# Kernel optimization log

Hardware: AMD Instinct MI355X
Metric: run time of the kernel (lower is better)

The kernel has to match this reference:

```python
import jax, jax.numpy as jnp
import numpy as np
from jax import lax

B, C_IN, C_OUT, H, W, K, PAD = 4, 64, 64, 96, 96, 3, 1
K2 = K * K


def setup_inputs() -> dict:
    key = jax.random.key(0)
    k1, k2, k3, k4, k5 = jax.random.split(key, 5)
    x = jax.random.normal(k1, (B, C_IN, H, W), jnp.float32)
    offset = jax.random.normal(k2, (B, 2 * K2, H, W), jnp.float32)
    weight = jax.random.normal(k3, (C_OUT, C_IN, K, K), jnp.float32) * 0.05
    mask_weight = jax.random.normal(k4, (K2, C_IN, K, K), jnp.float32) * 0.05
    mask_bias = jax.random.normal(k5, (K2,), jnp.float32) * 0.05
    return {"x": x, "offset": offset, "weight": weight,
            "mask_weight": mask_weight, "mask_bias": mask_bias}


def _deform_conv2d(x, offset, weight, mask):
    # torchvision ordering: per kernel tap k, offset[:, 2k] is dy, offset[:, 2k+1] is dx
    off_y = offset[:, 0::2]  # [B, K2, H, W]
    off_x = offset[:, 1::2]
    ky, kx = jnp.meshgrid(jnp.arange(K), jnp.arange(K), indexing="ij")
    ky = ky.reshape(K2).astype(x.dtype)
    kx = kx.reshape(K2).astype(x.dtype)
    hh = jnp.arange(H, dtype=x.dtype)
    ww = jnp.arange(W, dtype=x.dtype)
    base_y = hh[None, :, None] - PAD + ky[:, None, None]   # [K2, H, 1]
    base_x = ww[None, None, :] - PAD + kx[:, None, None]   # [K2, 1, W]
    py = base_y[None] + off_y                               # [B, K2, H, W]
    px = base_x[None] + off_x

    y0 = jnp.floor(py)
    x0 = jnp.floor(px)
    wy = py - y0   # bilinear weights
    wx = px - x0
    y0i = y0.astype(jnp.int32)
    x0i = x0.astype(jnp.int32)

    x_flat = x.reshape(B, C_IN, H * W)

    def gather(yy, xx):
        valid = (yy >= 0) & (yy < H) & (xx >= 0) & (xx < W)
        idx = jnp.clip(yy, 0, H - 1) * W + jnp.clip(xx, 0, W - 1)  # [B,K2,H,W]
        idx_f = idx.reshape(B, -1)
        v = jax.vmap(lambda xf, i: xf[:, i])(x_flat, idx_f)  # [B, C, K2*H*W]
        v = v.reshape(B, C_IN, K2, H, W)
        return v * valid[:, None].astype(v.dtype)

    v00 = gather(y0i, x0i)
    v01 = gather(y0i, x0i + 1)
    v10 = gather(y0i + 1, x0i)
    v11 = gather(y0i + 1, x0i + 1)

    wy_ = wy[:, None]  # [B,1,K2,H,W]
    wx_ = wx[:, None]
    sampled = (v00 * (1 - wy_) * (1 - wx_) + v01 * (1 - wy_) * wx_
               + v10 * wy_ * (1 - wx_) + v11 * wy_ * wx_)
    sampled = sampled * mask[:, None]  # modulate by sigmoid mask

    w2 = weight.reshape(C_OUT, C_IN, K2)
    return jnp.einsum("bckhw,ock->bohw", sampled, w2)


def reference(x, offset, weight, mask_weight, mask_bias):
    mask_logits = lax.conv_general_dilated(
        x, mask_weight, window_strides=(1, 1), padding=[(PAD, PAD), (PAD, PAD)],
        dimension_numbers=("NCHW", "OIHW", "NCHW"))
    mask = jax.nn.sigmoid(mask_logits + mask_bias[None, :, None, None])
    return _deform_conv2d(x, offset, weight, mask)
```

## Files before the change

### kernel.cpp

```cpp
#include <hip/hip_runtime.h>
#include <math.h>

#define BB 4
#define CI 64
#define CO 64
#define HH 96
#define WW 96
#define HW (HH*WW)
#define K2 9
#define PADC 1

#define TW 8
#define TH 4
#define TPXT (TW*TH)
#define TBX (WW/TW)
#define TBY (HH/TH)
#define NTILB (TBX*TBY)
#define NTILES (BB*NTILB)

#define WR (TH+9)
#define WC 20
#define SREC 72
#define NSLOT (WR*WC)

typedef __attribute__((ext_vector_type(8))) short short8;
typedef __attribute__((ext_vector_type(4))) float float4v;

#define WF_USHORTS (18*64*32)
#define MWF_USHORTS (18*16*32)

__device__ __forceinline__ float bf2f(short s) {
    return __uint_as_float(((unsigned int)(unsigned short)s) << 16);
}
__device__ __forceinline__ short f2bf(float f) {
    unsigned int u = __float_as_uint(f);
    u = (u + 0x7fffu + ((u >> 16) & 1u)) >> 16;
    return (short)u;
}

__device__ __forceinline__ void unswz(int bid, int* b, int* ty, int* tx) {
    int g = bid & 7, r = bid >> 3;
    *b = g & 3;
    int tile = (g >> 2) * 144 + r;
    *ty = tile / TBX; *tx = tile % TBX;
}

__global__ __launch_bounds__(256) void pack_kernel(const float* __restrict__ wgt,
                                                   const float* __restrict__ mw,
                                                   unsigned short* __restrict__ Wf,
                                                   unsigned short* __restrict__ MWf) {
    int i = blockIdx.x * 256 + threadIdx.x;
    if (i < WF_USHORTS) {
        int frag = i >> 11;
        int o = (i >> 5) & 63;
        int tt = i & 31;
        int k = frag >> 1, cc = frag & 1;
        int c = cc * 32 + tt;
        Wf[i] = (unsigned short)f2bf(wgt[o * 576 + c * 9 + k]);
    } else if (i < WF_USHORTS + MWF_USHORTS) {
        int e = i - WF_USHORTS;
        int frag = e >> 9;
        int m = (e >> 5) & 15;
        int tt = e & 31;
        int q = frag >> 1, cc = frag & 1;
        int c = cc * 32 + tt;
        MWf[e] = (m < 9) ? (unsigned short)f2bf(mw[m * 576 + c * 9 + q]) : 0;
    }
}

__global__ __launch_bounds__(256, 3) void fused_kernel(const float* __restrict__ x,
                                                       const float* __restrict__ off,
                                                       const float* __restrict__ mbias,
                                                       const unsigned short* __restrict__ Wf,
                                                       const unsigned short* __restrict__ MWf,
                                                       float* __restrict__ out) {
    __shared__ __align__(16) unsigned short win[NSLOT * SREC];
    __shared__ float s_mred[2][K2][TPXT];
    __shared__ int   s_idx[K2][4][TPXT];
    __shared__ float s_w[K2][4][TPXT];
    float* part = (float*)win;

    int t = threadIdx.x;
    int lane = t & 63, wv = t >> 6;
    int pg = wv >> 1, ch = wv & 1;
    int n = lane & 15, quad = lane >> 4;
    int b, ty, tx; unswz(blockIdx.x, &b, &ty, &tx);
    int h0 = ty * TH, w0 = tx * TW;
    int wr0 = h0 - 4, wc0 = w0 - 4;
    const float* xb = x + (size_t)b * CI * HW;

    for (int e = t; e < WR * 32 * 5; e += 256) {
        int r = e / 160, rem = e % 160, chp = rem / 5, c4 = rem % 5;
        int row = min(max(wr0 + r, 0), HH - 1);
        int c0c = wc0 + c4 * 4;
        const float* s0 = xb + (size_t)(2 * chp) * HW + row * WW;
        const float* s1 = s0 + HW;
        float v0[4], v1[4];
        if (c0c >= 0 && c0c + 3 < WW) {
            float4v a = *(const float4v*)(s0 + c0c);
            float4v bq = *(const float4v*)(s1 + c0c);
            v0[0]=a[0]; v0[1]=a[1]; v0[2]=a[2]; v0[3]=a[3];
            v1[0]=bq[0]; v1[1]=bq[1]; v1[2]=bq[2]; v1[3]=bq[3];
        } else {
            #pragma unroll
            for (int j = 0; j < 4; j++) {
                int cc2 = min(max(c0c + j, 0), WW - 1);
                v0[j] = s0[cc2]; v1[j] = s1[cc2];
            }
        }
        #pragma unroll
        for (int j = 0; j < 4; j++) {
            unsigned int pk = (unsigned short)f2bf(v0[j]) |
                              ((unsigned int)(unsigned short)f2bf(v1[j]) << 16);
            *(unsigned int*)&win[(r * WC + c4 * 4 + j) * SREC + 2 * chp] = pk;
        }
    }
    __syncthreads();

    int pxl = pg * 16 + n;
    int ly = pxl >> 3, lx = pxl & 7;
    int h = h0 + ly, wcc = w0 + lx;
    int cbase_us = ch * 32 + quad * 8;

    {
        float4v macc = {0.f, 0.f, 0.f, 0.f};
        #pragma unroll
        for (int q = 0; q < 9; q++) {
            int hh = h + q / 3 - 1, ww2 = wcc + q % 3 - 1;
            bool valid = (hh >= 0) && (hh < HH) && (ww2 >= 0) && (ww2 < WW);
            short8 bfrag = {0, 0, 0, 0, 0, 0, 0, 0};
            if (valid) {
                int slot = (hh - wr0) * WC + (ww2 - wc0);
                bfrag = *(const short8*)&win[slot * SREC + cbase_us];
            }
            short8 afrag = *(const short8*)(MWf + ((size_t)((q * 2 + ch) * 16 + n)) * 32 + quad * 8);
            macc = __builtin_amdgcn_mfma_f32_16x16x32_bf16(afrag, bfrag, macc, 0, 0, 0);
        }
        #pragma unroll
        for (int r = 0; r < 4; r++) {
            int row = quad * 4 + r;
            if (row < 9) s_mred[ch][row][pxl] = macc[r];
        }
    }
    __syncthreads();

    for (int e = t; e < K2 * TPXT; e += 256) {
        int k = e >> 5, pe = e & 31;
        int ph = h0 + (pe >> 3), pw = w0 + (pe & 7);
        int p = ph * WW + pw;
        float oy = off[((size_t)b * 2 * K2 + 2 * k) * HW + p];
        float ox = off[((size_t)b * 2 * K2 + 2 * k + 1) * HW + p];
        float s = s_mred[0][k][pe] + s_mred[1][k][pe] + mbias[k];
        float m = 1.f / (1.f + expf(-s));
        float py  = (float)(ph - PADC + k / 3) + oy;
        float pxf = (float)(pw - PADC + k % 3) + ox;
        float y0f = floorf(py), x0f = floorf(pxf);
        float wy = py - y0f, wx = pxf - x0f;
        int y0 = (int)y0f, x0 = (int)x0f;
        int y1 = y0 + 1, x1 = x0 + 1;
        int y0c = min(max(y0, 0), HH - 1), y1c = min(max(y1, 0), HH - 1);
        int x0c = min(max(x0, 0), WW - 1), x1c = min(max(x1, 0), WW - 1);
        bool vy0 = (y0 >= 0) && (y0 < HH), vy1 = (y1 >= 0) && (y1 < HH);
        bool vx0 = (x0 >= 0) && (x0 < WW), vx1 = (x1 >= 0) && (x1 < WW);
        float w00 = (1.f - wy) * (1.f - wx) * m; if (!(vy0 && vx0)) w00 = 0.f;
        float w01 = (1.f - wy) * wx * m;         if (!(vy0 && vx1)) w01 = 0.f;
        float w10 = wy * (1.f - wx) * m;         if (!(vy1 && vx0)) w10 = 0.f;
        float w11 = wy * wx * m;                 if (!(vy1 && vx1)) w11 = 0.f;
        s_idx[k][0][pe] = (y0c << 16) | x0c;
        s_idx[k][1][pe] = (y0c << 16) | x1c;
        s_idx[k][2][pe] = (y1c << 16) | x0c;
        s_idx[k][3][pe] = (y1c << 16) | x1c;
        s_w[k][0][pe] = w00; s_w[k][1][pe] = w01;
        s_w[k][2][pe] = w10; s_w[k][3][pe] = w11;
    }
    __syncthreads();

    float4v acc0 = {0.f, 0.f, 0.f, 0.f};
    float4v acc1 = {0.f, 0.f, 0.f, 0.f};
    float4v acc2 = {0.f, 0.f, 0.f, 0.f};
    float4v acc3 = {0.f, 0.f, 0.f, 0.f};
    const float* xfb = xb + (size_t)(ch * 32 + quad * 8) * HW;

    #pragma unroll
    for (int k = 0; k < 9; k++) {
        short8 U[4];
        #pragma unroll
        for (int cor = 0; cor < 4; cor++) {
            int yx = s_idx[k][cor][pxl];
            int yy = yx >> 16, xx = yx & 0xffff;
            int r = yy - wr0, c = xx - wc0;
            bool inw = ((unsigned)r < (unsigned)WR) && ((unsigned)c < (unsigned)WC);
            short8 u;
            if (inw) {
                u = *(const short8*)&win[(r * WC + c) * SREC + cbase_us];
            } else {
                const float* fs = xfb + yy * WW + xx;
                #pragma unroll
                for (int j = 0; j < 8; j++) u[j] = f2bf(fs[(size_t)j * HW]);
            }
            U[cor] = u;
        }
        float w0 = s_w[k][0][pxl], w1 = s_w[k][1][pxl];
        float w2 = s_w[k][2][pxl], w3 = s_w[k][3][pxl];
        short8 bfrag;
        #pragma unroll
        for (int j = 0; j < 8; j++) {
            float v = bf2f(U[0][j]) * w0 + bf2f(U[1][j]) * w1 +
                      bf2f(U[2][j]) * w2 + bf2f(U[3][j]) * w3;
            bfrag[j] = f2bf(v);
        }
        const unsigned short* wp = Wf + (size_t)((k * 2 + ch) * 64) * 32 + quad * 8;
        short8 a0 = *(const short8*)(wp + (0 * 16 + n) * 32);
        short8 a1 = *(const short8*)(wp + (1 * 16 + n) * 32);
        short8 a2 = *(const short8*)(wp + (2 * 16 + n) * 32);
        short8 a3 = *(const short8*)(wp + (3 * 16 + n) * 32);
        acc0 = __builtin_amdgcn_mfma_f32_16x16x32_bf16(a0, bfrag, acc0, 0, 0, 0);
        acc1 = __builtin_amdgcn_mfma_f32_16x16x32_bf16(a1, bfrag, acc1, 0, 0, 0);
        acc2 = __builtin_amdgcn_mfma_f32_16x16x32_bf16(a2, bfrag, acc2, 0, 0, 0);
        acc3 = __builtin_amdgcn_mfma_f32_16x16x32_bf16(a3, bfrag, acc3, 0, 0, 0);
    }

    __syncthreads();
    if (ch == 1) {
        #pragma unroll
        for (int r = 0; r < 4; r++) {
            part[(pg * 16 + 0 * 4 + r) * 64 + lane] = acc0[r];
            part[(pg * 16 + 1 * 4 + r) * 64 + lane] = acc1[r];
            part[(pg * 16 + 2 * 4 + r) * 64 + lane] = acc2[r];
            part[(pg * 16 + 3 * 4 + r) * 64 + lane] = acc3[r];
        }
    }
    __syncthreads();
    if (ch == 0) {
        float* ob = out + (size_t)b * CO * HW + h * WW + wcc;
        #pragma unroll
        for (int r = 0; r < 4; r++) {
            ob[(size_t)(0 * 16 + quad * 4 + r) * HW] =
                acc0[r] + part[(pg * 16 + 0 * 4 + r) * 64 + lane];
            ob[(size_t)(1 * 16 + quad * 4 + r) * HW] =
                acc1[r] + part[(pg * 16 + 1 * 4 + r) * 64 + lane];
            ob[(size_t)(2 * 16 + quad * 4 + r) * HW] =
                acc2[r] + part[(pg * 16 + 2 * 4 + r) * 64 + lane];
            ob[(size_t)(3 * 16 + quad * 4 + r) * HW] =
                acc3[r] + part[(pg * 16 + 3 * 4 + r) * 64 + lane];
        }
    }
}

extern "C" void kernel_launch(void* const* d_in, const int* in_sizes, int n_in,
                              void* d_out, int out_size, void* d_ws, size_t ws_size,
                              hipStream_t stream) {
    const float* x   = (const float*)d_in[0];
    const float* off = (const float*)d_in[1];
    const float* wgt = (const float*)d_in[2];
    const float* mw  = (const float*)d_in[3];
    const float* mb  = (const float*)d_in[4];
    float* out = (float*)d_out;

    unsigned short* Wf  = (unsigned short*)d_ws;
    unsigned short* MWf = Wf + WF_USHORTS;

    hipLaunchKernelGGL(pack_kernel, dim3((WF_USHORTS + MWF_USHORTS + 255) / 256), dim3(256),
                       0, stream, wgt, mw, Wf, MWf);
    hipLaunchKernelGGL(fused_kernel, dim3(NTILES), dim3(256), 0, stream,
                       x, off, mb, Wf, MWf, out);
}
```

Measured before the change: 101.2 us.

## Persistent grid with register-resident weights and tap-split waves on smaller tiles

Result: slower. 115.2 us (+13.8%).

```diff
diff --git a/kernel.cpp b/kernel.cpp
--- a/kernel.cpp
+++ b/kernel.cpp
@@ -10,18 +10,20 @@
 #define K2 9
 #define PADC 1
 
-#define TW 8
+#define TW 4
 #define TH 4
 #define TPXT (TW*TH)
 #define TBX (WW/TW)
 #define TBY (HH/TH)
 #define NTILB (TBX*TBY)
 #define NTILES (BB*NTILB)
-
-#define WR (TH+9)
-#define WC 20
+#define GRID 512
+
+#define WR 13
+#define WC 16
 #define SREC 72
 #define NSLOT (WR*WC)
+#define STASKS (WR*32*4)
 
 typedef __attribute__((ext_vector_type(8))) short short8;
 typedef __attribute__((ext_vector_type(4))) float float4v;
@@ -38,10 +40,10 @@
     return (short)u;
 }
 
-__device__ __forceinline__ void unswz(int bid, int* b, int* ty, int* tx) {
-    int g = bid & 7, r = bid >> 3;
+__device__ __forceinline__ void unswz(int tt, int* b, int* ty, int* tx) {
+    int g = tt & 7, r = tt >> 3;
     *b = g & 3;
-    int tile = (g >> 2) * 144 + r;
+    int tile = (g >> 2) * 288 + r;
     *ty = tile / TBX; *tx = tile % TBX;
 }
 
@@ -68,183 +70,218 @@
     }
 }
 
-__global__ __launch_bounds__(256, 3) void fused_kernel(const float* __restrict__ x,
+struct SmemT {
+    unsigned short win[NSLOT * SREC];
+    float mred[2][2][K2][TPXT];
+    int   idx[K2][4][TPXT];
+    float w[K2][4][TPXT];
+};
+
+template<int KB, int KE>
+__device__ __forceinline__ void run_tiles(SmemT& sm, int t, int wv, int ch, int tg,
+                                          const float* __restrict__ x,
+                                          const float* __restrict__ off,
+                                          const float* __restrict__ mbias,
+                                          const unsigned short* __restrict__ Wf,
+                                          const unsigned short* __restrict__ MWf,
+                                          float* __restrict__ out, int bid) {
+    constexpr int NK = KE - KB;
+    int lane = t & 63;
+    int n = lane & 15, quad = lane >> 4;
+    float* part = (float*)sm.win;
+
+    short8 wA[NK][4];
+    short8 mA[NK];
+    #pragma unroll
+    for (int kk = 0; kk < NK; kk++) {
+        int k = KB + kk;
+        const unsigned short* wp = Wf + (size_t)((k * 2 + ch) * 64) * 32 + quad * 8;
+        #pragma unroll
+        for (int s = 0; s < 4; s++)
+            wA[kk][s] = *(const short8*)(wp + (s * 16 + n) * 32);
+        mA[kk] = *(const short8*)(MWf + ((size_t)((k * 2 + ch) * 16 + n)) * 32 + quad * 8);
+    }
+
+    int ly = n >> 2, lx = n & 3;
+    int cbase_us = ch * 32 + quad * 8;
+
+    for (int tt = bid; tt < NTILES; tt += GRID) {
+        int b, ty, tx; unswz(tt, &b, &ty, &tx);
+        int h0 = ty * TH, w0 = tx * TW;
+        int wr0 = h0 - 4, wc0 = w0 - 4;
+        const float* xb = x + (size_t)b * CI * HW;
+        int h = h0 + ly, wcc = w0 + lx;
+
+        __syncthreads();
+
+        for (int e = t; e < STASKS; e += 256) {
+            int r = e >> 7;
+            int chp = (e >> 2) & 31;
+            int c4 = e & 3;
+            int row = min(max(wr0 + r, 0), HH - 1);
+            int c0c = wc0 + c4 * 4;
+            const float* s0 = xb + (size_t)(2 * chp) * HW + row * WW;
+            const float* s1 = s0 + HW;
+            float v0[4], v1[4];
+            if (c0c >= 0 && c0c + 3 < WW) {
+                float4v a = *(const float4v*)(s0 + c0c);
+                float4v bq = *(const float4v*)(s1 + c0c);
+                v0[0]=a[0]; v0[1]=a[1]; v0[2]=a[2]; v0[3]=a[3];
+                v1[0]=bq[0]; v1[1]=bq[1]; v1[2]=bq[2]; v1[3]=bq[3];
+            } else {
+                #pragma unroll
+                for (int j = 0; j < 4; j++) {
+                    int cc2 = min(max(c0c + j, 0), WW - 1);
+                    v0[j] = s0[cc2]; v1[j] = s1[cc2];
+                }
+            }
+            #pragma unroll
+            for (int j = 0; j < 4; j++) {
+                unsigned int pk = (unsigned short)f2bf(v0[j]) |
+                                  ((unsigned int)(unsigned short)f2bf(v1[j]) << 16);
+                *(unsigned int*)&sm.win[(r * WC + c4 * 4 + j) * SREC + 2 * chp] = pk;
+            }
+        }
+        __syncthreads();
+
+        {
+            float4v macc = {0.f, 0.f, 0.f, 0.f};
+            #pragma unroll
+            for (int kk = 0; kk < NK; kk++) {
+                int q = KB + kk;
+                int hh = h + q / 3 - 1, ww2 = wcc + q % 3 - 1;
+                bool valid = (hh >= 0) && (hh < HH) && (ww2 >= 0) && (ww2 < WW);
+                short8 bfrag = {0, 0, 0, 0, 0, 0, 0, 0};
+                if (valid) {
+                    int slot = (hh - wr0) * WC + (ww2 - wc0);
+                    bfrag = *(const short8*)&sm.win[slot * SREC + cbase_us];
+                }
+                macc = __builtin_amdgcn_mfma_f32_16x16x32_bf16(mA[kk], bfrag, macc, 0, 0, 0);
+            }
+            #pragma unroll
+            for (int r = 0; r < 4; r++) {
+                int row = quad * 4 + r;
+                if (row < 9) sm.mred[ch][tg][row][n] = macc[r];
+            }
+        }
+        __syncthreads();
+
+        if (t < K2 * TPXT) {
+            int k = t >> 4, pe = t & 15;
+            int ph = h0 + (pe >> 2), pw = w0 + (pe & 3);
+            int p = ph * WW + pw;
+            float oy = off[((size_t)b * 2 * K2 + 2 * k) * HW + p];
+            float ox = off[((size_t)b * 2 * K2 + 2 * k + 1) * HW + p];
+            float s = sm.mred[0][0][k][pe] + sm.mred[0][1][k][pe] +
+                      sm.mred[1][0][k][pe] + sm.mred[1][1][k][pe] + mbias[k];
+            float m = 1.f / (1.f + expf(-s));
+            float py  = (float)(ph - PADC + k / 3) + oy;
+            float pxf = (float)(pw - PADC + k % 3) + ox;
+            float y0f = floorf(py), x0f = floorf(pxf);
+            float wy = py - y0f, wx = pxf - x0f;
+            int y0 = (int)y0f, x0 = (int)x0f;
+            int y1 = y0 + 1, x1 = x0 + 1;
+            int y0c = min(max(y0, 0), HH - 1), y1c = min(max(y1, 0), HH - 1);
+            int x0c = min(max(x0, 0), WW - 1), x1c = min(max(x1, 0), WW - 1);
+            bool vy0 = (y0 >= 0) && (y0 < HH), vy1 = (y1 >= 0) && (y1 < HH);
+            bool vx0 = (x0 >= 0) && (x0 < WW), vx1 = (x1 >= 0) && (x1 < WW);
+            float w00 = (1.f - wy) * (1.f - wx) * m; if (!(vy0 && vx0)) w00 = 0.f;
+            float w01 = (1.f - wy) * wx * m;         if (!(vy0 && vx1)) w01 = 0.f;
+            float w10 = wy * (1.f - wx) * m;         if (!(vy1 && vx0)) w10 = 0.f;
+            float w11 = wy * wx * m;                 if (!(vy1 && vx1)) w11 = 0.f;
+            sm.idx[k][0][pe] = (y0c << 16) | x0c;
+            sm.idx[k][1][pe] = (y0c << 16) | x1c;
+            sm.idx[k][2][pe] = (y1c << 16) | x0c;
+            sm.idx[k][3][pe] = (y1c << 16) | x1c;
+            sm.w[k][0][pe] = w00; sm.w[k][1][pe] = w01;
+            sm.w[k][2][pe] = w10; sm.w[k][3][pe] = w11;
+        }
+        __syncthreads();
+
+        float4v acc0 = {0.f, 0.f, 0.f, 0.f};
+        float4v acc1 = {0.f, 0.f, 0.f, 0.f};
+        float4v acc2 = {0.f, 0.f, 0.f, 0.f};
+        float4v acc3 = {0.f, 0.f, 0.f, 0.f};
+        const float* xfb = xb + (size_t)(ch * 32 + quad * 8) * HW;
+
+        #pragma unroll
+        for (int kk = 0; kk < NK; kk++) {
+            int k = KB + kk;
+            short8 U[4];
+            #pragma unroll
+            for (int cor = 0; cor < 4; cor++) {
+                int yx = sm.idx[k][cor][n];
+                int yy = yx >> 16, xx = yx & 0xffff;
+                int r = yy - wr0, c = xx - wc0;
+                bool inw = ((unsigned)r < (unsigned)WR) && ((unsigned)c < (unsigned)WC);
+                short8 u;
+                if (inw) {
+                    u = *(const short8*)&sm.win[(r * WC + c) * SREC + cbase_us];
+                } else {
+                    const float* fs = xfb + yy * WW + xx;
+                    #pragma unroll
+                    for (int j = 0; j < 8; j++) u[j] = f2bf(fs[(size_t)j * HW]);
+                }
+                U[cor] = u;
+            }
+            float w0 = sm.w[k][0][n], w1 = sm.w[k][1][n];
+            float w2 = sm.w[k][2][n], w3 = sm.w[k][3][n];
+            short8 bfrag;
+            #pragma unroll
+            for (int j = 0; j < 8; j++) {
+                float v = bf2f(U[0][j]) * w0 + bf2f(U[1][j]) * w1 +
+                          bf2f(U[2][j]) * w2 + bf2f(U[3][j]) * w3;
+                bfrag[j] = f2bf(v);
+            }
+            acc0 = __builtin_amdgcn_mfma_f32_16x16x32_bf16(wA[kk][0], bfrag, acc0, 0, 0, 0);
+            acc1 = __builtin_amdgcn_mfma_f32_16x16x32_bf16(wA[kk][1], bfrag, acc1, 0, 0, 0);
+            acc2 = __builtin_amdgcn_mfma_f32_16x16x32_bf16(wA[kk][2], bfrag, acc2, 0, 0, 0);
+            acc3 = __builtin_amdgcn_mfma_f32_16x16x32_bf16(wA[kk][3], bfrag, acc3, 0, 0, 0);
+        }
+
+        __syncthreads();
+        if (wv != 0) {
+            #pragma unroll
+            for (int r = 0; r < 4; r++) {
+                part[((wv - 1) * 16 + 0 * 4 + r) * 64 + lane] = acc0[r];
+                part[((wv - 1) * 16 + 1 * 4 + r) * 64 + lane] = acc1[r];
+                part[((wv - 1) * 16 + 2 * 4 + r) * 64 + lane] = acc2[r];
+                part[((wv - 1) * 16 + 3 * 4 + r) * 64 + lane] = acc3[r];
+            }
+        }
+        __syncthreads();
+        if (wv == 0) {
+            float* ob = out + (size_t)b * CO * HW + h * WW + wcc;
+            #pragma unroll
+            for (int r = 0; r < 4; r++) {
+                int j0 = r, j1 = 4 + r, j2 = 8 + r, j3 = 12 + r;
+                ob[(size_t)(0 * 16 + quad * 4 + r) * HW] = acc0[r] +
+                    part[j0 * 64 + lane] + part[(16 + j0) * 64 + lane] + part[(32 + j0) * 64 + lane];
+                ob[(size_t)(1 * 16 + quad * 4 + r) * HW] = acc1[r] +
+                    part[j1 * 64 + lane] + part[(16 + j1) * 64 + lane] + part[(32 + j1) * 64 + lane];
+                ob[(size_t)(2 * 16 + quad * 4 + r) * HW] = acc2[r] +
+                    part[j2 * 64 + lane] + part[(16 + j2) * 64 + lane] + part[(32 + j2) * 64 + lane];
+                ob[(size_t)(3 * 16 + quad * 4 + r) * HW] = acc3[r] +
+                    part[j3 * 64 + lane] + part[(16 + j3) * 64 + lane] + part[(32 + j3) * 64 + lane];
+            }
+        }
+    }
+}
+
+__global__ __launch_bounds__(256, 2) void fused_kernel(const float* __restrict__ x,
                                                        const float* __restrict__ off,
                                                        const float* __restrict__ mbias,
                                                        const unsigned short* __restrict__ Wf,
                                                        const unsigned short* __restrict__ MWf,
                                                        float* __restrict__ out) {
-    __shared__ __align__(16) unsigned short win[NSLOT * SREC];
-    __shared__ float s_mred[2][K2][TPXT];
-    __shared__ int   s_idx[K2][4][TPXT];
-    __shared__ float s_w[K2][4][TPXT];
-    float* part = (float*)win;
-
+    __shared__ SmemT sm;
     int t = threadIdx.x;
-    int lane = t & 63, wv = t >> 6;
-    int pg = wv >> 1, ch = wv & 1;
-    int n = lane & 15, quad = lane >> 4;
-    int b, ty, tx; unswz(blockIdx.x, &b, &ty, &tx);
-    int h0 = ty * TH, w0 = tx * TW;
-    int wr0 = h0 - 4, wc0 = w0 - 4;
-    const float* xb = x + (size_t)b * CI * HW;
-
-    for (int e = t; e < WR * 32 * 5; e += 256) {
-        int r = e / 160, rem = e % 160, chp = rem / 5, c4 = rem % 5;
-        int row = min(max(wr0 + r, 0), HH - 1);
-        int c0c = wc0 + c4 * 4;
-        const float* s0 = xb + (size_t)(2 * chp) * HW + row * WW;
-        const float* s1 = s0 + HW;
-        float v0[4], v1[4];
-        if (c0c >= 0 && c0c + 3 < WW) {
-            float4v a = *(const float4v*)(s0 + c0c);
-            float4v bq = *(const float4v*)(s1 + c0c);
-            v0[0]=a[0]; v0[1]=a[1]; v0[2]=a[2]; v0[3]=a[3];
-            v1[0]=bq[0]; v1[1]=bq[1]; v1[2]=bq[2]; v1[3]=bq[3];
-        } else {
-            #pragma unroll
-            for (int j = 0; j < 4; j++) {
-                int cc2 = min(max(c0c + j, 0), WW - 1);
-                v0[j] = s0[cc2]; v1[j] = s1[cc2];
-            }
-        }
-        #pragma unroll
-        for (int j = 0; j < 4; j++) {
-            unsigned int pk = (unsigned short)f2bf(v0[j]) |
-                              ((unsigned int)(unsigned short)f2bf(v1[j]) << 16);
-            *(unsigned int*)&win[(r * WC + c4 * 4 + j) * SREC + 2 * chp] = pk;
-        }
-    }
-    __syncthreads();
-
-    int pxl = pg * 16 + n;
-    int ly = pxl >> 3, lx = pxl & 7;
-    int h = h0 + ly, wcc = w0 + lx;
-    int cbase_us = ch * 32 + quad * 8;
-
-    {
-        float4v macc = {0.f, 0.f, 0.f, 0.f};
-        #pragma unroll
-        for (int q = 0; q < 9; q++) {
-            int hh = h + q / 3 - 1, ww2 = wcc + q % 3 - 1;
-            bool valid = (hh >= 0) && (hh < HH) && (ww2 >= 0) && (ww2 < WW);
-            short8 bfrag = {0, 0, 0, 0, 0, 0, 0, 0};
-            if (valid) {
-                int slot = (hh - wr0) * WC + (ww2 - wc0);
-                bfrag = *(const short8*)&win[slot * SREC + cbase_us];
-            }
-            short8 afrag = *(const short8*)(MWf + ((size_t)((q * 2 + ch) * 16 + n)) * 32 + quad * 8);
-            macc = __builtin_amdgcn_mfma_f32_16x16x32_bf16(afrag, bfrag, macc, 0, 0, 0);
-        }
-        #pragma unroll
-        for (int r = 0; r < 4; r++) {
-            int row = quad * 4 + r;
-            if (row < 9) s_mred[ch][row][pxl] = macc[r];
-        }
-    }
-    __syncthreads();
-
-    for (int e = t; e < K2 * TPXT; e += 256) {
-        int k = e >> 5, pe = e & 31;
-        int ph = h0 + (pe >> 3), pw = w0 + (pe & 7);
-        int p = ph * WW + pw;
-        float oy = off[((size_t)b * 2 * K2 + 2 * k) * HW + p];
-        float ox = off[((size_t)b * 2 * K2 + 2 * k + 1) * HW + p];
-        float s = s_mred[0][k][pe] + s_mred[1][k][pe] + mbias[k];
-        float m = 1.f / (1.f + expf(-s));
-        float py  = (float)(ph - PADC + k / 3) + oy;
-        float pxf = (float)(pw - PADC + k % 3) + ox;
-        float y0f = floorf(py), x0f = floorf(pxf);
-        float wy = py - y0f, wx = pxf - x0f;
-        int y0 = (int)y0f, x0 = (int)x0f;
-        int y1 = y0 + 1, x1 = x0 + 1;
-        int y0c = min(max(y0, 0), HH - 1), y1c = min(max(y1, 0), HH - 1);
-        int x0c = min(max(x0, 0), WW - 1), x1c = min(max(x1, 0), WW - 1);
-        bool vy0 = (y0 >= 0) && (y0 < HH), vy1 = (y1 >= 0) && (y1 < HH);
-        bool vx0 = (x0 >= 0) && (x0 < WW), vx1 = (x1 >= 0) && (x1 < WW);
-        float w00 = (1.f - wy) * (1.f - wx) * m; if (!(vy0 && vx0)) w00 = 0.f;
-        float w01 = (1.f - wy) * wx * m;         if (!(vy0 && vx1)) w01 = 0.f;
-        float w10 = wy * (1.f - wx) * m;         if (!(vy1 && vx0)) w10 = 0.f;
-        float w11 = wy * wx * m;                 if (!(vy1 && vx1)) w11 = 0.f;
-        s_idx[k][0][pe] = (y0c << 16) | x0c;
-        s_idx[k][1][pe] = (y0c << 16) | x1c;
-        s_idx[k][2][pe] = (y1c << 16) | x0c;
-        s_idx[k][3][pe] = (y1c << 16) | x1c;
-        s_w[k][0][pe] = w00; s_w[k][1][pe] = w01;
-        s_w[k][2][pe] = w10; s_w[k][3][pe] = w11;
-    }
-    __syncthreads();
-
-    float4v acc0 = {0.f, 0.f, 0.f, 0.f};
-    float4v acc1 = {0.f, 0.f, 0.f, 0.f};
-    float4v acc2 = {0.f, 0.f, 0.f, 0.f};
-    float4v acc3 = {0.f, 0.f, 0.f, 0.f};
-    const float* xfb = xb + (size_t)(ch * 32 + quad * 8) * HW;
-
-    #pragma unroll
-    for (int k = 0; k < 9; k++) {
-        short8 U[4];
-        #pragma unroll
-        for (int cor = 0; cor < 4; cor++) {
-            int yx = s_idx[k][cor][pxl];
-            int yy = yx >> 16, xx = yx & 0xffff;
-            int r = yy - wr0, c = xx - wc0;
-            bool inw = ((unsigned)r < (unsigned)WR) && ((unsigned)c < (unsigned)WC);
-            short8 u;
-            if (inw) {
-                u = *(const short8*)&win[(r * WC + c) * SREC + cbase_us];
-            } else {
-                const float* fs = xfb + yy * WW + xx;
-                #pragma unroll
-                for (int j = 0; j < 8; j++) u[j] = f2bf(fs[(size_t)j * HW]);
-            }
-            U[cor] = u;
-        }
-        float w0 = s_w[k][0][pxl], w1 = s_w[k][1][pxl];
-        float w2 = s_w[k][2][pxl], w3 = s_w[k][3][pxl];
-        short8 bfrag;
-        #pragma unroll
-        for (int j = 0; j < 8; j++) {
-            float v = bf2f(U[0][j]) * w0 + bf2f(U[1][j]) * w1 +
-                      bf2f(U[2][j]) * w2 + bf2f(U[3][j]) * w3;
-            bfrag[j] = f2bf(v);
-        }
-        const unsigned short* wp = Wf + (size_t)((k * 2 + ch) * 64) * 32 + quad * 8;
-        short8 a0 = *(const short8*)(wp + (0 * 16 + n) * 32);
-        short8 a1 = *(const short8*)(wp + (1 * 16 + n) * 32);
-        short8 a2 = *(const short8*)(wp + (2 * 16 + n) * 32);
-        short8 a3 = *(const short8*)(wp + (3 * 16 + n) * 32);
-        acc0 = __builtin_amdgcn_mfma_f32_16x16x32_bf16(a0, bfrag, acc0, 0, 0, 0);
-        acc1 = __builtin_amdgcn_mfma_f32_16x16x32_bf16(a1, bfrag, acc1, 0, 0, 0);
-        acc2 = __builtin_amdgcn_mfma_f32_16x16x32_bf16(a2, bfrag, acc2, 0, 0, 0);
-        acc3 = __builtin_amdgcn_mfma_f32_16x16x32_bf16(a3, bfrag, acc3, 0, 0, 0);
-    }
-
-    __syncthreads();
-    if (ch == 1) {
-        #pragma unroll
-        for (int r = 0; r < 4; r++) {
-            part[(pg * 16 + 0 * 4 + r) * 64 + lane] = acc0[r];
-            part[(pg * 16 + 1 * 4 + r) * 64 + lane] = acc1[r];
-            part[(pg * 16 + 2 * 4 + r) * 64 + lane] = acc2[r];
-            part[(pg * 16 + 3 * 4 + r) * 64 + lane] = acc3[r];
-        }
-    }
-    __syncthreads();
-    if (ch == 0) {
-        float* ob = out + (size_t)b * CO * HW + h * WW + wcc;
-        #pragma unroll
-        for (int r = 0; r < 4; r++) {
-            ob[(size_t)(0 * 16 + quad * 4 + r) * HW] =
-                acc0[r] + part[(pg * 16 + 0 * 4 + r) * 64 + lane];
-            ob[(size_t)(1 * 16 + quad * 4 + r) * HW] =
-                acc1[r] + part[(pg * 16 + 1 * 4 + r) * 64 + lane];
-            ob[(size_t)(2 * 16 + quad * 4 + r) * HW] =
-                acc2[r] + part[(pg * 16 + 2 * 4 + r) * 64 + lane];
-            ob[(size_t)(3 * 16 + quad * 4 + r) * HW] =
-                acc3[r] + part[(pg * 16 + 3 * 4 + r) * 64 + lane];
-        }
-    }
+    int wv = t >> 6;
+    int ch = wv & 1, tg = wv >> 1;
+    if (tg == 0)
+        run_tiles<0, 5>(sm, t, wv, ch, tg, x, off, mbias, Wf, MWf, out, blockIdx.x);
+    else
+        run_tiles<5, 9>(sm, t, wv, ch, tg, x, off, mbias, Wf, MWf, out, blockIdx.x);
 }
 
 extern "C" void kernel_launch(void* const* d_in, const int* in_sizes, int n_in,
@@ -262,6 +299,6 @@
 
     hipLaunchKernelGGL(pack_kernel, dim3((WF_USHORTS + MWF_USHORTS + 255) / 256), dim3(256),
                        0, stream, wgt, mw, Wf, MWf);
-    hipLaunchKernelGGL(fused_kernel, dim3(NTILES), dim3(256), 0, stream,
+    hipLaunchKernelGGL(fused_kernel, dim3(GRID), dim3(256), 0, stream,
                        x, off, mb, Wf, MWf, out);
 }
```
